# Kernel tuning notes

Hardware: AMD Instinct MI355X
Metric: run time of the kernel (lower is better)

The kernel has to match this reference:

```python
import jax, jax.numpy as jnp
import numpy as np

INPUT_DIM = 1024
OUTPUT_DIM = 1024


def setup_inputs() -> dict:
    key = jax.random.key(0)
    k1, k2, k3, k4 = jax.random.split(key, 4)
    B, S, D = 4, 2048, INPUT_DIM
    src = jax.random.normal(k1, (B, S, D), dtype=jnp.float32)
    tgt = jax.random.normal(k2, (B, S, D), dtype=jnp.float32)
    # nn.Linear(input_dim*2, output_dim): weight [out, in], bias [out]
    bound = 1.0 / np.sqrt(2 * D)
    W = jax.random.uniform(k3, (OUTPUT_DIM, 2 * D), jnp.float32, -bound, bound)
    b = jax.random.uniform(k4, (OUTPUT_DIM,), jnp.float32, -bound, bound)
    return {"src": src, "tgt": tgt, "W": W, "b": b}


def reference(src, tgt, W, b):
    # weight = bmm(tgt, src^T): [B, S_tgt, S_src]
    weight = jnp.einsum("btd,bsd->bts", tgt, src)
    # NOTE: original uses Softmax(dim=1) -> normalizes over the tgt axis
    weight = jax.nn.softmax(weight, axis=1)
    # weighted sum over src positions: [B, S_tgt, D]
    weight_sum = jnp.einsum("bts,bsd->btd", weight, src)
    output = jnp.concatenate([weight_sum, tgt], axis=2)  # [B, S_tgt, 2D]
    output = output @ W.T + b  # [B, S_tgt, output_dim]
    return (output, weight)
```

## Files before the change

### kernel.cpp

```cpp
#include <hip/hip_runtime.h>
#include <stdint.h>


#define B_   4
#define S_   2048
#define D_   1024
#define OUTD 1024
#define K2   2048

typedef unsigned short ushort_t;
typedef _Float16 half8 __attribute__((ext_vector_type(8)));
typedef float    f32x4 __attribute__((ext_vector_type(4)));

__device__ __forceinline__ ushort_t f2h(float f) {
    union { _Float16 h; ushort_t u; } v;
    v.h = (_Float16)f;
    return v.u;
}
__device__ __forceinline__ float h2f(ushort_t u) {
    union { _Float16 h; ushort_t u; } v;
    v.u = u;
    return (float)v.h;
}

__device__ __forceinline__ void ld16(const ushort_t* g, ushort_t* l) {
    __builtin_amdgcn_global_load_lds(
        (const __attribute__((address_space(1))) void*)g,
        (__attribute__((address_space(3))) void*)l, 16, 0, 0);
}


__global__ void k_split(const float4* __restrict__ src, const float4* __restrict__ tgt,
                        ushort4* __restrict__ sh,
                        ushort4* __restrict__ th, ushort4* __restrict__ tl,
                        ushort4* __restrict__ acat)
{
    const int64_t n4 = (int64_t)B_ * S_ * D_ / 4;
    for (int64_t i = (int64_t)blockIdx.x * blockDim.x + threadIdx.x; i < n4;
         i += (int64_t)gridDim.x * blockDim.x) {
        float4 s = src[i];
        sh[i] = (ushort4){f2h(s.x), f2h(s.y), f2h(s.z), f2h(s.w)};
        float4 tv = tgt[i];
        ushort4 ht = {f2h(tv.x), f2h(tv.y), f2h(tv.z), f2h(tv.w)};
        th[i] = ht;
        tl[i] = (ushort4){f2h(tv.x - h2f(ht.x)), f2h(tv.y - h2f(ht.y)),
                          f2h(tv.z - h2f(ht.z)), f2h(tv.w - h2f(ht.w))};
        int64_t row = i >> 8;
        acat[row * 512 + 256 + (i & 255)] = ht;
    }
}

__global__ void k_wconv(const float4* __restrict__ W, ushort4* __restrict__ wb)
{
    const int64_t n4 = (int64_t)OUTD * K2 / 4;
    for (int64_t i = (int64_t)blockIdx.x * blockDim.x + threadIdx.x; i < n4;
         i += (int64_t)gridDim.x * blockDim.x) {
        float4 w = W[i];
        wb[i] = (ushort4){f2h(w.x), f2h(w.y), f2h(w.z), f2h(w.w)};
    }
}

__global__ void k_transpose(const float* __restrict__ src, ushort_t* __restrict__ sT)
{
    __shared__ ushort_t tile[32][33];
    int b  = blockIdx.z;
    int d0 = blockIdx.x * 32, s0 = blockIdx.y * 32;
    int tx = threadIdx.x, ty = threadIdx.y;
#pragma unroll
    for (int i = 0; i < 4; i++) {
        int s = s0 + ty + i * 8;
        tile[ty + i * 8][tx] = f2h(src[((int64_t)b * S_ + s) * D_ + d0 + tx]);
    }
    __syncthreads();
#pragma unroll
    for (int i = 0; i < 4; i++) {
        int d = d0 + ty + i * 8;
        sT[((int64_t)b * D_ + d) * S_ + s0 + tx] = tile[tx][ty + i * 8];
    }
}

__launch_bounds__(256)
__global__ void k_gemm_logits(const ushort_t* __restrict__ Ah, const ushort_t* __restrict__ Al,
                              const ushort_t* __restrict__ Bs,
                              float* __restrict__ C,
                              float* __restrict__ pm, float* __restrict__ ps)
{
    const int M = S_, N = S_, K = D_;
    int b = blockIdx.z;
    Ah += (int64_t)b * M * K;  Al += (int64_t)b * M * K;
    Bs += (int64_t)b * N * K;
    C  += (int64_t)b * M * N;

    __shared__ __align__(16) ushort_t sAh[128 * 32], sAl[128 * 32], sB[128 * 32];
    __shared__ float red_m[2][128], red_s[2][128];

    int t    = threadIdx.x;
    int m0   = blockIdx.y * 128, n0 = blockIdx.x * 128;
    int wave = t >> 6, lane = t & 63;
    int wr   = (wave >> 1) * 64, wc = (wave & 1) * 64;
    int l15  = lane & 15, quad = lane >> 4;

    f32x4 acc[4][4];
#pragma unroll
    for (int i = 0; i < 4; i++)
#pragma unroll
        for (int j = 0; j < 4; j++) acc[i][j] = (f32x4){0.f, 0.f, 0.f, 0.f};

    int srow = t >> 2;
    int scol = (t & 3) * 8;

    const ushort_t* gAh0 = Ah + (int64_t)(m0 + srow) * K + scol;
    const ushort_t* gAh1 = gAh0 + (int64_t)64 * K;
    const ushort_t* gAl0 = Al + (int64_t)(m0 + srow) * K + scol;
    const ushort_t* gAl1 = gAl0 + (int64_t)64 * K;
    const ushort_t* gB0  = Bs + (int64_t)(n0 + srow) * K + scol;
    const ushort_t* gB1  = gB0 + (int64_t)64 * K;

    ushort_t* lAh0 = sAh + wave * 512;  ushort_t* lAh1 = sAh + 2048 + wave * 512;
    ushort_t* lAl0 = sAl + wave * 512;  ushort_t* lAl1 = sAl + 2048 + wave * 512;
    ushort_t* lB0  = sB  + wave * 512;  ushort_t* lB1  = sB  + 2048 + wave * 512;

    for (int k0 = 0; k0 < K; k0 += 32) {
        ld16(gAh0, lAh0);  ld16(gAh1, lAh1);
        ld16(gAl0, lAl0);  ld16(gAl1, lAl1);
        ld16(gB0,  lB0);   ld16(gB1,  lB1);
        gAh0 += 32; gAh1 += 32; gAl0 += 32; gAl1 += 32; gB0 += 32; gB1 += 32;
        __syncthreads();

        half8 ah[4], al[4], bf[4];
#pragma unroll
        for (int i = 0; i < 4; i++) {
            ah[i] = *(const half8*)(&sAh[(wr + i * 16 + l15) * 32 + quad * 8]);
            al[i] = *(const half8*)(&sAl[(wr + i * 16 + l15) * 32 + quad * 8]);
        }
#pragma unroll
        for (int j = 0; j < 4; j++)
            bf[j] = *(const half8*)(&sB[(wc + j * 16 + l15) * 32 + quad * 8]);
#pragma unroll
        for (int i = 0; i < 4; i++)
#pragma unroll
            for (int j = 0; j < 4; j++) {
                acc[i][j] = __builtin_amdgcn_mfma_f32_16x16x32_f16(ah[i], bf[j], acc[i][j], 0, 0, 0);
                acc[i][j] = __builtin_amdgcn_mfma_f32_16x16x32_f16(al[i], bf[j], acc[i][j], 0, 0, 0);
            }
        __syncthreads();
    }

#pragma unroll
    for (int i = 0; i < 4; i++) {
        int row_base = m0 + wr + i * 16 + quad * 4;
#pragma unroll
        for (int j = 0; j < 4; j++) {
            int col = n0 + wc + j * 16 + l15;
#pragma unroll
            for (int r = 0; r < 4; r++)
                C[(int64_t)(row_base + r) * N + col] = acc[i][j][r];
        }
    }

    int rowhalf = wave >> 1;
#pragma unroll
    for (int j = 0; j < 4; j++) {
        float m = -3.0e38f;
#pragma unroll
        for (int i = 0; i < 4; i++)
#pragma unroll
            for (int r = 0; r < 4; r++) m = fmaxf(m, acc[i][j][r]);
        float s = 0.f;
#pragma unroll
        for (int i = 0; i < 4; i++)
#pragma unroll
            for (int r = 0; r < 4; r++) s += __expf(acc[i][j][r] - m);
#pragma unroll
        for (int d = 16; d <= 32; d <<= 1) {
            float m2 = __shfl_xor(m, d, 64);
            float s2 = __shfl_xor(s, d, 64);
            float nm = fmaxf(m, m2);
            s = s * __expf(m - nm) + s2 * __expf(m2 - nm);
            m = nm;
        }
        if (lane < 16) {
            red_m[rowhalf][wc + j * 16 + l15] = m;
            red_s[rowhalf][wc + j * 16 + l15] = s;
        }
    }
    __syncthreads();
    if (t < 128) {
        float ma = red_m[0][t], mb = red_m[1][t];
        float sa = red_s[0][t], sb = red_s[1][t];
        float m = fmaxf(ma, mb);
        float s = sa * __expf(ma - m) + sb * __expf(mb - m);
        int idx = blockIdx.y * (B_ * S_) + b * S_ + n0 + t;
        pm[idx] = m;
        ps[idx] = s;
    }
}


__global__ void k_colstats2(const float* __restrict__ pm, const float* __restrict__ ps,
                            float* __restrict__ cmax, float* __restrict__ cinv)
{
    int i = blockIdx.x * 256 + threadIdx.x;
    float m = -3.0e38f;
#pragma unroll
    for (int c = 0; c < 16; c++) m = fmaxf(m, pm[c * (B_ * S_) + i]);
    float sum = 0.f;
#pragma unroll
    for (int c = 0; c < 16; c++) sum += ps[c * (B_ * S_) + i] * __expf(pm[c * (B_ * S_) + i] - m);
    cmax[i] = m;
    cinv[i] = 1.0f / sum;
}

__global__ void k_softmax_norm(float4* __restrict__ L, const float4* __restrict__ cmax4,
                               const float4* __restrict__ cinv4, ushort4* __restrict__ wbf)
{
    const int64_t n4 = (int64_t)B_ * S_ * S_ / 4;
    for (int64_t i = (int64_t)blockIdx.x * blockDim.x + threadIdx.x; i < n4;
         i += (int64_t)gridDim.x * blockDim.x) {
        int b  = (int)(i >> 20);
        int c4 = (int)(i & 511);
        float4 x  = L[i];
        float4 cm = cmax4[b * 512 + c4];
        float4 ci = cinv4[b * 512 + c4];
        float4 w;
        w.x = __expf(x.x - cm.x) * ci.x;
        w.y = __expf(x.y - cm.y) * ci.y;
        w.z = __expf(x.z - cm.z) * ci.z;
        w.w = __expf(x.w - cm.w) * ci.w;
        L[i] = w;
        wbf[i] = (ushort4){f2h(w.x), f2h(w.y), f2h(w.z), f2h(w.w)};
    }
}

__launch_bounds__(256)
__global__ void k_gemm_wsum(const ushort_t* __restrict__ Wt, const ushort_t* __restrict__ Bt,
                            ushort_t* __restrict__ acat)
{
    const int M = S_, N = D_, K = S_;
    int b = blockIdx.z;
    const ushort_t* A  = Wt + (int64_t)b * M * K;
    const ushort_t* Bm = Bt + (int64_t)b * N * K;

    __shared__ __align__(16) ushort_t sA[128 * 32], sB[128 * 32];

    int t    = threadIdx.x;
    int m0   = blockIdx.y * 128, n0 = blockIdx.x * 128;
    int wave = t >> 6, lane = t & 63;
    int wr   = (wave >> 1) * 64, wc = (wave & 1) * 64;
    int l15  = lane & 15, quad = lane >> 4;

    f32x4 acc[4][4];
#pragma unroll
    for (int i = 0; i < 4; i++)
#pragma unroll
        for (int j = 0; j < 4; j++) acc[i][j] = (f32x4){0.f, 0.f, 0.f, 0.f};

    int srow = t >> 2, scol = (t & 3) * 8;

    const ushort_t* gA0 = A  + (int64_t)(m0 + srow) * K + scol;
    const ushort_t* gA1 = gA0 + (int64_t)64 * K;
    const ushort_t* gB0 = Bm + (int64_t)(n0 + srow) * K + scol;
    const ushort_t* gB1 = gB0 + (int64_t)64 * K;
    ushort_t* lA0 = sA + wave * 512;  ushort_t* lA1 = sA + 2048 + wave * 512;
    ushort_t* lB0 = sB + wave * 512;  ushort_t* lB1 = sB + 2048 + wave * 512;

    for (int k0 = 0; k0 < K; k0 += 32) {
        ld16(gA0, lA0);  ld16(gA1, lA1);
        ld16(gB0, lB0);  ld16(gB1, lB1);
        gA0 += 32; gA1 += 32; gB0 += 32; gB1 += 32;
        __syncthreads();

        half8 af[4], bf[4];
#pragma unroll
        for (int i = 0; i < 4; i++) af[i] = *(const half8*)(&sA[(wr + i * 16 + l15) * 32 + quad * 8]);
#pragma unroll
        for (int j = 0; j < 4; j++) bf[j] = *(const half8*)(&sB[(wc + j * 16 + l15) * 32 + quad * 8]);
#pragma unroll
        for (int i = 0; i < 4; i++)
#pragma unroll
            for (int j = 0; j < 4; j++)
                acc[i][j] = __builtin_amdgcn_mfma_f32_16x16x32_f16(af[i], bf[j], acc[i][j], 0, 0, 0);
        __syncthreads();
    }

#pragma unroll
    for (int i = 0; i < 4; i++) {
        int row_base = m0 + wr + i * 16 + quad * 4;
#pragma unroll
        for (int j = 0; j < 4; j++) {
            int col = n0 + wc + j * 16 + l15;
#pragma unroll
            for (int r = 0; r < 4; r++)
                acat[((int64_t)b * S_ + row_base + r) * K2 + col] = f2h(acc[i][j][r]);
        }
    }
}

__launch_bounds__(256)
__global__ void k_gemm_out(const ushort_t* __restrict__ A, const ushort_t* __restrict__ Bw,
                           const float* __restrict__ bias, float* __restrict__ out)
{
    const int N = OUTD, K = K2;

    __shared__ __align__(16) ushort_t sA[128 * 32], sB[128 * 32];

    int t    = threadIdx.x;
    int m0   = blockIdx.y * 128, n0 = blockIdx.x * 128;
    int wave = t >> 6, lane = t & 63;
    int wr   = (wave >> 1) * 64, wc = (wave & 1) * 64;
    int l15  = lane & 15, quad = lane >> 4;

    f32x4 acc[4][4];
#pragma unroll
    for (int i = 0; i < 4; i++)
#pragma unroll
        for (int j = 0; j < 4; j++) acc[i][j] = (f32x4){0.f, 0.f, 0.f, 0.f};

    int srow = t >> 2, scol = (t & 3) * 8;

    const ushort_t* gA0 = A  + (int64_t)(m0 + srow) * K + scol;
    const ushort_t* gA1 = gA0 + (int64_t)64 * K;
    const ushort_t* gB0 = Bw + (int64_t)(n0 + srow) * K + scol;
    const ushort_t* gB1 = gB0 + (int64_t)64 * K;
    ushort_t* lA0 = sA + wave * 512;  ushort_t* lA1 = sA + 2048 + wave * 512;
    ushort_t* lB0 = sB + wave * 512;  ushort_t* lB1 = sB + 2048 + wave * 512;

    for (int k0 = 0; k0 < K; k0 += 32) {
        ld16(gA0, lA0);  ld16(gA1, lA1);
        ld16(gB0, lB0);  ld16(gB1, lB1);
        gA0 += 32; gA1 += 32; gB0 += 32; gB1 += 32;
        __syncthreads();

        half8 af[4], bf[4];
#pragma unroll
        for (int i = 0; i < 4; i++) af[i] = *(const half8*)(&sA[(wr + i * 16 + l15) * 32 + quad * 8]);
#pragma unroll
        for (int j = 0; j < 4; j++) bf[j] = *(const half8*)(&sB[(wc + j * 16 + l15) * 32 + quad * 8]);
#pragma unroll
        for (int i = 0; i < 4; i++)
#pragma unroll
            for (int j = 0; j < 4; j++)
                acc[i][j] = __builtin_amdgcn_mfma_f32_16x16x32_f16(af[i], bf[j], acc[i][j], 0, 0, 0);
        __syncthreads();
    }

#pragma unroll
    for (int i = 0; i < 4; i++) {
        int row_base = m0 + wr + i * 16 + quad * 4;
#pragma unroll
        for (int j = 0; j < 4; j++) {
            int col = n0 + wc + j * 16 + l15;
            float bv = bias[col];
#pragma unroll
            for (int r = 0; r < 4; r++)
                out[(int64_t)(row_base + r) * N + col] = acc[i][j][r] + bv;
        }
    }
}


extern "C" void kernel_launch(void* const* d_in, const int* in_sizes, int n_in,
                              void* d_out, int out_size, void* d_ws, size_t ws_size,
                              hipStream_t stream)
{
    const float* src  = (const float*)d_in[0];
    const float* tgt  = (const float*)d_in[1];
    const float* W    = (const float*)d_in[2];
    const float* bias = (const float*)d_in[3];

    float* out = (float*)d_out;
    float* Lw  = out + (size_t)B_ * S_ * OUTD;

    char*  ws = (char*)d_ws;
    size_t o  = 0;
    auto take = [&](size_t bytes) -> char* {
        char* p = ws + o;
        o += (bytes + 255) & ~(size_t)255;
        return p;
    };
    const size_t ELEMS = (size_t)B_ * S_ * D_;
    ushort_t* sh   = (ushort_t*)take(ELEMS * 2);
    ushort_t* th   = (ushort_t*)take(ELEMS * 2);
    ushort_t* tl   = (ushort_t*)take(ELEMS * 2);
    ushort_t* sT   = (ushort_t*)take(ELEMS * 2);
    ushort_t* wbf  = (ushort_t*)take((size_t)B_ * S_ * S_ * 2);
    ushort_t* acat = (ushort_t*)take((size_t)B_ * S_ * K2 * 2);
    ushort_t* wb   = (ushort_t*)take((size_t)OUTD * K2 * 2);
    float*    pm   = (float*)take(16 * (size_t)B_ * S_ * 4);
    float*    ps   = (float*)take(16 * (size_t)B_ * S_ * 4);
    float*    cmax = (float*)take((size_t)B_ * S_ * 4);
    float*    cinv = (float*)take((size_t)B_ * S_ * 4);
    (void)ws_size; (void)in_sizes; (void)n_in; (void)out_size;

    k_split<<<dim3(2048), dim3(256), 0, stream>>>((const float4*)src, (const float4*)tgt,
                                                  (ushort4*)sh, (ushort4*)th, (ushort4*)tl,
                                                  (ushort4*)acat);
    k_wconv<<<dim3(512), dim3(256), 0, stream>>>((const float4*)W, (ushort4*)wb);
    k_transpose<<<dim3(32, 64, 4), dim3(32, 8), 0, stream>>>(src, sT);

    k_gemm_logits<<<dim3(16, 16, 4), dim3(256), 0, stream>>>(th, tl, sh, Lw, pm, ps);

    k_colstats2<<<dim3(32), dim3(256), 0, stream>>>(pm, ps, cmax, cinv);
    k_softmax_norm<<<dim3(2048), dim3(256), 0, stream>>>((float4*)Lw, (const float4*)cmax,
                                                         (const float4*)cinv, (ushort4*)wbf);

    k_gemm_wsum<<<dim3(8, 16, 4), dim3(256), 0, stream>>>(wbf, sT, acat);
    k_gemm_out<<<dim3(8, 64), dim3(256), 0, stream>>>(acat, wb, bias, out);
}
```

Measured before the change: 389.9 us.

## Reassociate output projection through attention weights and drop transpose/concat buffers

Splits the output linear layer into src and tgt halves. It precomputes W1·srcᵀ and tgt·W2ᵀ with a generic NT fp16 GEMM, then applies the attention weights directly to the projected src and adds the tgt term and bias in the final epilogue. This removes the src transpose kernel, the concatenated intermediate buffer and the separate output GEMM. GEMM k-tiles are widened to 64 to halve the barrier count. The projected intermediate is rounded to fp16, which adds some precision loss.

```diff
diff --git a/kernel.cpp b/kernel.cpp
--- a/kernel.cpp
+++ b/kernel.cpp
@@ -6,7 +6,6 @@
 #define S_   2048
 #define D_   1024
 #define OUTD 1024
-#define K2   2048
 
 typedef unsigned short ushort_t;
 typedef _Float16 half8 __attribute__((ext_vector_type(8)));
@@ -32,8 +31,7 @@
 
 __global__ void k_split(const float4* __restrict__ src, const float4* __restrict__ tgt,
                         ushort4* __restrict__ sh,
-                        ushort4* __restrict__ th, ushort4* __restrict__ tl,
-                        ushort4* __restrict__ acat)
+                        ushort4* __restrict__ th, ushort4* __restrict__ tl)
 {
     const int64_t n4 = (int64_t)B_ * S_ * D_ / 4;
     for (int64_t i = (int64_t)blockIdx.x * blockDim.x + threadIdx.x; i < n4;
@@ -45,37 +43,16 @@
         th[i] = ht;
         tl[i] = (ushort4){f2h(tv.x - h2f(ht.x)), f2h(tv.y - h2f(ht.y)),
                           f2h(tv.z - h2f(ht.z)), f2h(tv.w - h2f(ht.w))};
-        int64_t row = i >> 8;
-        acat[row * 512 + 256 + (i & 255)] = ht;
     }
 }
 
 __global__ void k_wconv(const float4* __restrict__ W, ushort4* __restrict__ wb)
 {
-    const int64_t n4 = (int64_t)OUTD * K2 / 4;
+    const int64_t n4 = (int64_t)OUTD * 2 * D_ / 4;
     for (int64_t i = (int64_t)blockIdx.x * blockDim.x + threadIdx.x; i < n4;
          i += (int64_t)gridDim.x * blockDim.x) {
         float4 w = W[i];
         wb[i] = (ushort4){f2h(w.x), f2h(w.y), f2h(w.z), f2h(w.w)};
-    }
-}
-
-__global__ void k_transpose(const float* __restrict__ src, ushort_t* __restrict__ sT)
-{
-    __shared__ ushort_t tile[32][33];
-    int b  = blockIdx.z;
-    int d0 = blockIdx.x * 32, s0 = blockIdx.y * 32;
-    int tx = threadIdx.x, ty = threadIdx.y;
-#pragma unroll
-    for (int i = 0; i < 4; i++) {
-        int s = s0 + ty + i * 8;
-        tile[ty + i * 8][tx] = f2h(src[((int64_t)b * S_ + s) * D_ + d0 + tx]);
-    }
-    __syncthreads();
-#pragma unroll
-    for (int i = 0; i < 4; i++) {
-        int d = d0 + ty + i * 8;
-        sT[((int64_t)b * D_ + d) * S_ + s0 + tx] = tile[tx][ty + i * 8];
     }
 }
 
@@ -233,15 +210,16 @@
 }
 
 __launch_bounds__(256)
-__global__ void k_gemm_wsum(const ushort_t* __restrict__ Wt, const ushort_t* __restrict__ Bt,
-                            ushort_t* __restrict__ acat)
-{
-    const int M = S_, N = D_, K = S_;
+__global__ void k_gemm_nt_f16(const ushort_t* __restrict__ A, int lda, int64_t bsA,
+                              const ushort_t* __restrict__ Bm, int ldb, int64_t bsB,
+                              ushort_t* __restrict__ C, int ldc, int64_t bsC, int K)
+{
     int b = blockIdx.z;
-    const ushort_t* A  = Wt + (int64_t)b * M * K;
-    const ushort_t* Bm = Bt + (int64_t)b * N * K;
-
-    __shared__ __align__(16) ushort_t sA[128 * 32], sB[128 * 32];
+    A  += (int64_t)b * bsA;
+    Bm += (int64_t)b * bsB;
+    C  += (int64_t)b * bsC;
+
+    __shared__ __align__(16) ushort_t sA[128 * 64], sB[128 * 64];
 
     int t    = threadIdx.x;
     int m0   = blockIdx.y * 128, n0 = blockIdx.x * 128;
@@ -255,31 +233,36 @@
 #pragma unroll
         for (int j = 0; j < 4; j++) acc[i][j] = (f32x4){0.f, 0.f, 0.f, 0.f};
 
-    int srow = t >> 2, scol = (t & 3) * 8;
-
-    const ushort_t* gA0 = A  + (int64_t)(m0 + srow) * K + scol;
-    const ushort_t* gA1 = gA0 + (int64_t)64 * K;
-    const ushort_t* gB0 = Bm + (int64_t)(n0 + srow) * K + scol;
-    const ushort_t* gB1 = gB0 + (int64_t)64 * K;
-    ushort_t* lA0 = sA + wave * 512;  ushort_t* lA1 = sA + 2048 + wave * 512;
-    ushort_t* lB0 = sB + wave * 512;  ushort_t* lB1 = sB + 2048 + wave * 512;
-
-    for (int k0 = 0; k0 < K; k0 += 32) {
-        ld16(gA0, lA0);  ld16(gA1, lA1);
-        ld16(gB0, lB0);  ld16(gB1, lB1);
-        gA0 += 32; gA1 += 32; gB0 += 32; gB1 += 32;
-        __syncthreads();
-
-        half8 af[4], bf[4];
-#pragma unroll
-        for (int i = 0; i < 4; i++) af[i] = *(const half8*)(&sA[(wr + i * 16 + l15) * 32 + quad * 8]);
-#pragma unroll
-        for (int j = 0; j < 4; j++) bf[j] = *(const half8*)(&sB[(wc + j * 16 + l15) * 32 + quad * 8]);
-#pragma unroll
-        for (int i = 0; i < 4; i++)
+    int srow = t >> 3;
+    int scol = (t & 7) * 8;
+
+    const ushort_t* gA = A  + (int64_t)(m0 + srow) * lda + scol;
+    const ushort_t* gB = Bm + (int64_t)(n0 + srow) * ldb + scol;
+    ushort_t* lA = sA + wave * 512;
+    ushort_t* lB = sB + wave * 512;
+
+    for (int k0 = 0; k0 < K; k0 += 64) {
+#pragma unroll
+        for (int j = 0; j < 4; j++) {
+            ld16(gA + (int64_t)(j * 32) * lda + k0, lA + j * 2048);
+            ld16(gB + (int64_t)(j * 32) * ldb + k0, lB + j * 2048);
+        }
+        __syncthreads();
+#pragma unroll
+        for (int ks = 0; ks < 64; ks += 32) {
+            half8 af[4], bf[4];
+#pragma unroll
+            for (int i = 0; i < 4; i++)
+                af[i] = *(const half8*)(&sA[(wr + i * 16 + l15) * 64 + ks + quad * 8]);
 #pragma unroll
             for (int j = 0; j < 4; j++)
-                acc[i][j] = __builtin_amdgcn_mfma_f32_16x16x32_f16(af[i], bf[j], acc[i][j], 0, 0, 0);
+                bf[j] = *(const half8*)(&sB[(wc + j * 16 + l15) * 64 + ks + quad * 8]);
+#pragma unroll
+            for (int i = 0; i < 4; i++)
+#pragma unroll
+                for (int j = 0; j < 4; j++)
+                    acc[i][j] = __builtin_amdgcn_mfma_f32_16x16x32_f16(af[i], bf[j], acc[i][j], 0, 0, 0);
+        }
         __syncthreads();
     }
 
@@ -291,18 +274,24 @@
             int col = n0 + wc + j * 16 + l15;
 #pragma unroll
             for (int r = 0; r < 4; r++)
-                acat[((int64_t)b * S_ + row_base + r) * K2 + col] = f2h(acc[i][j][r]);
+                C[(int64_t)(row_base + r) * ldc + col] = f2h(acc[i][j][r]);
         }
     }
 }
 
 __launch_bounds__(256)
-__global__ void k_gemm_out(const ushort_t* __restrict__ A, const ushort_t* __restrict__ Bw,
-                           const float* __restrict__ bias, float* __restrict__ out)
-{
-    const int N = OUTD, K = K2;
-
-    __shared__ __align__(16) ushort_t sA[128 * 32], sB[128 * 32];
+__global__ void k_gemm_final(const ushort_t* __restrict__ Wt, const ushort_t* __restrict__ PT,
+                             const ushort_t* __restrict__ Q, const float* __restrict__ bias,
+                             float* __restrict__ out)
+{
+    const int K = S_, N = OUTD;
+    int b = blockIdx.z;
+    const ushort_t* A  = Wt + (int64_t)b * S_ * S_;
+    const ushort_t* Bm = PT + (int64_t)b * OUTD * S_;
+    const ushort_t* Qb = Q  + (int64_t)b * S_ * OUTD;
+    float* Cb = out + (int64_t)b * S_ * OUTD;
+
+    __shared__ __align__(16) ushort_t sA[128 * 64], sB[128 * 64];
 
     int t    = threadIdx.x;
     int m0   = blockIdx.y * 128, n0 = blockIdx.x * 128;
@@ -316,31 +305,36 @@
 #pragma unroll
         for (int j = 0; j < 4; j++) acc[i][j] = (f32x4){0.f, 0.f, 0.f, 0.f};
 
-    int srow = t >> 2, scol = (t & 3) * 8;
-
-    const ushort_t* gA0 = A  + (int64_t)(m0 + srow) * K + scol;
-    const ushort_t* gA1 = gA0 + (int64_t)64 * K;
-    const ushort_t* gB0 = Bw + (int64_t)(n0 + srow) * K + scol;
-    const ushort_t* gB1 = gB0 + (int64_t)64 * K;
-    ushort_t* lA0 = sA + wave * 512;  ushort_t* lA1 = sA + 2048 + wave * 512;
-    ushort_t* lB0 = sB + wave * 512;  ushort_t* lB1 = sB + 2048 + wave * 512;
-
-    for (int k0 = 0; k0 < K; k0 += 32) {
-        ld16(gA0, lA0);  ld16(gA1, lA1);
-        ld16(gB0, lB0);  ld16(gB1, lB1);
-        gA0 += 32; gA1 += 32; gB0 += 32; gB1 += 32;
-        __syncthreads();
-
-        half8 af[4], bf[4];
-#pragma unroll
-        for (int i = 0; i < 4; i++) af[i] = *(const half8*)(&sA[(wr + i * 16 + l15) * 32 + quad * 8]);
-#pragma unroll
-        for (int j = 0; j < 4; j++) bf[j] = *(const half8*)(&sB[(wc + j * 16 + l15) * 32 + quad * 8]);
-#pragma unroll
-        for (int i = 0; i < 4; i++)
+    int srow = t >> 3;
+    int scol = (t & 7) * 8;
+
+    const ushort_t* gA = A  + (int64_t)(m0 + srow) * K + scol;
+    const ushort_t* gB = Bm + (int64_t)(n0 + srow) * K + scol;
+    ushort_t* lA = sA + wave * 512;
+    ushort_t* lB = sB + wave * 512;
+
+    for (int k0 = 0; k0 < K; k0 += 64) {
+#pragma unroll
+        for (int j = 0; j < 4; j++) {
+            ld16(gA + (int64_t)(j * 32) * K + k0, lA + j * 2048);
+            ld16(gB + (int64_t)(j * 32) * K + k0, lB + j * 2048);
+        }
+        __syncthreads();
+#pragma unroll
+        for (int ks = 0; ks < 64; ks += 32) {
+            half8 af[4], bf[4];
+#pragma unroll
+            for (int i = 0; i < 4; i++)
+                af[i] = *(const half8*)(&sA[(wr + i * 16 + l15) * 64 + ks + quad * 8]);
 #pragma unroll
             for (int j = 0; j < 4; j++)
-                acc[i][j] = __builtin_amdgcn_mfma_f32_16x16x32_f16(af[i], bf[j], acc[i][j], 0, 0, 0);
+                bf[j] = *(const half8*)(&sB[(wc + j * 16 + l15) * 64 + ks + quad * 8]);
+#pragma unroll
+            for (int i = 0; i < 4; i++)
+#pragma unroll
+                for (int j = 0; j < 4; j++)
+                    acc[i][j] = __builtin_amdgcn_mfma_f32_16x16x32_f16(af[i], bf[j], acc[i][j], 0, 0, 0);
+        }
         __syncthreads();
     }
 
@@ -352,8 +346,10 @@
             int col = n0 + wc + j * 16 + l15;
             float bv = bias[col];
 #pragma unroll
-            for (int r = 0; r < 4; r++)
-                out[(int64_t)(row_base + r) * N + col] = acc[i][j][r] + bv;
+            for (int r = 0; r < 4; r++) {
+                int64_t idx = (int64_t)(row_base + r) * N + col;
+                Cb[idx] = acc[i][j][r] + h2f(Qb[idx]) + bv;
+            }
         }
     }
 }
@@ -382,10 +378,10 @@
     ushort_t* sh   = (ushort_t*)take(ELEMS * 2);
     ushort_t* th   = (ushort_t*)take(ELEMS * 2);
     ushort_t* tl   = (ushort_t*)take(ELEMS * 2);
-    ushort_t* sT   = (ushort_t*)take(ELEMS * 2);
     ushort_t* wbf  = (ushort_t*)take((size_t)B_ * S_ * S_ * 2);
-    ushort_t* acat = (ushort_t*)take((size_t)B_ * S_ * K2 * 2);
-    ushort_t* wb   = (ushort_t*)take((size_t)OUTD * K2 * 2);
+    ushort_t* wb   = (ushort_t*)take((size_t)OUTD * 2 * D_ * 2);
+    ushort_t* PT   = (ushort_t*)take((size_t)B_ * OUTD * S_ * 2);
+    ushort_t* Qb   = (ushort_t*)take((size_t)B_ * S_ * OUTD * 2);
     float*    pm   = (float*)take(16 * (size_t)B_ * S_ * 4);
     float*    ps   = (float*)take(16 * (size_t)B_ * S_ * 4);
     float*    cmax = (float*)take((size_t)B_ * S_ * 4);
@@ -393,10 +389,18 @@
     (void)ws_size; (void)in_sizes; (void)n_in; (void)out_size;
 
     k_split<<<dim3(2048), dim3(256), 0, stream>>>((const float4*)src, (const float4*)tgt,
-                                                  (ushort4*)sh, (ushort4*)th, (ushort4*)tl,
-                                                  (ushort4*)acat);
+                                                  (ushort4*)sh, (ushort4*)th, (ushort4*)tl);
     k_wconv<<<dim3(512), dim3(256), 0, stream>>>((const float4*)W, (ushort4*)wb);
-    k_transpose<<<dim3(32, 64, 4), dim3(32, 8), 0, stream>>>(src, sT);
+
+    k_gemm_nt_f16<<<dim3(16, 8, 4), dim3(256), 0, stream>>>(
+        wb, 2 * D_, 0,
+        sh, D_, (int64_t)S_ * D_,
+        PT, S_, (int64_t)OUTD * S_, D_);
+
+    k_gemm_nt_f16<<<dim3(8, 16, 4), dim3(256), 0, stream>>>(
+        th, D_, (int64_t)S_ * D_,
+        wb + D_, 2 * D_, 0,
+        Qb, OUTD, (int64_t)S_ * OUTD, D_);
 
     k_gemm_logits<<<dim3(16, 16, 4), dim3(256), 0, stream>>>(th, tl, sh, Lw, pm, ps);
 
@@ -404,6 +408,5 @@
     k_softmax_norm<<<dim3(2048), dim3(256), 0, stream>>>((float4*)Lw, (const float4*)cmax,
                                                          (const float4*)cinv, (ushort4*)wbf);
 
-    k_gemm_wsum<<<dim3(8, 16, 4), dim3(256), 0, stream>>>(wbf, sT, acat);
-    k_gemm_out<<<dim3(8, 64), dim3(256), 0, stream>>>(acat, wb, bias, out);
-}
+    k_gemm_final<<<dim3(8, 16, 4), dim3(256), 0, stream>>>(wbf, PT, Qb, bias, out);
+}
```

Result: faster. 378.2 us (-3.0%).
